# Kernel optimization log

Measured on AMD Instinct MI355X. Metric: run time of the kernel, lower is better.

## Reference

```python
import jax, jax.numpy as jnp
import numpy as np

N = 1536
F = 64          # in_features
F_IN = F + 1    # include_adj adds adjacency channel
OUT = 64


def setup_inputs() -> dict:
    key = jax.random.key(0)
    k1, k2, k3, k4 = jax.random.split(key, 4)
    feat = jax.random.normal(k1, (N, F), dtype=jnp.float32)
    adj = jax.random.uniform(k2, (N, N), dtype=jnp.float32)
    # nn.Linear init: U(-1/sqrt(fan_in), 1/sqrt(fan_in))
    bound = 1.0 / np.sqrt(F_IN)
    W = jax.random.uniform(k3, (OUT, F_IN), minval=-bound, maxval=bound, dtype=jnp.float32)
    b = jax.random.uniform(k4, (OUT,), minval=-bound, maxval=bound, dtype=jnp.float32)
    return {"feat": feat, "adj": adj, "W": W, "b": b}


def reference(feat, adj, W, b):
    # pairwise abs-diff via broadcasting (no repeat): [N, N, F]
    feat_diff = jnp.abs(feat[None, :, :] - feat[:, None, :])
    # concat adjacency as extra channel -> [N, N, F+1], then flatten rows
    x = jnp.concatenate([feat_diff, adj[:, :, None]], axis=2).reshape(N * N, F_IN)
    # Linear: x @ W.T + b -> [N*N, OUT]
    return x @ W.T + b
```

## Files before the change

### kernel.cpp

```cpp
#include <hip/hip_runtime.h>
#include <hip/hip_bf16.h>

#define N_NODES 1536
#define NF 64
#define NOUT 64
#define FIN 65
#define TI 6

typedef __bf16 bf16x8 __attribute__((ext_vector_type(8)));
typedef float f32x4 __attribute__((ext_vector_type(4)));

__global__ __launch_bounds__(256, 4)
void edge_gcn_mfma(const float* __restrict__ feat,
                   const float* __restrict__ adj,
                   const float* __restrict__ W,
                   const float* __restrict__ b,
                   float* __restrict__ out)
{
    const int tid  = threadIdx.x;
    const int lane = tid & 63;
    const int wv   = tid >> 6;
    const int l15  = lane & 15;
    const int lg   = lane >> 4;

    const int i0 = blockIdx.y * TI;
    const int j0 = blockIdx.x * 128;
    const int jw = j0 + wv * 32;

    __shared__ float lds[8192];
    __shared__ float fslab[TI * NF];
    __shared__ float aslab[TI * 128];
    float* const lbase = lds + wv * 2048;

    if (tid < 96) {
        const int row = tid >> 4;
        const int col = (tid & 15) * 4;
        *reinterpret_cast<f32x4*>(&fslab[row * NF + col]) =
            *reinterpret_cast<const f32x4*>(
                &feat[(size_t)(i0 + row) * NF + col]);
    }
    if (tid < 192) {
        const int row = tid >> 5;
        const int col = (tid & 31) * 4;
        *reinterpret_cast<f32x4*>(&aslab[row * 128 + col]) =
            *reinterpret_cast<const f32x4*>(
                &adj[(size_t)(i0 + row) * N_NODES + j0 + col]);
    }

    bf16x8 afrag[2][4];
#pragma unroll
    for (int kk = 0; kk < 2; ++kk) {
#pragma unroll
        for (int mo = 0; mo < 4; ++mo) {
            const float* wp = W + (mo * 16 + l15) * FIN + kk * 32 + lg * 8;
#pragma unroll
            for (int e = 0; e < 8; ++e) afrag[kk][mo][e] = (__bf16)wp[e];
        }
    }

    bf16x8 fjrb[2][2];
#pragma unroll
    for (int n = 0; n < 2; ++n) {
        const float* fjrow = feat + (jw + n * 16 + l15) * NF;
#pragma unroll
        for (int kk = 0; kk < 2; ++kk)
#pragma unroll
            for (int e = 0; e < 8; ++e)
                fjrb[n][kk][e] = (__bf16)fjrow[kk * 32 + lg * 8 + e];
    }

    float wlB[4], bvB[4];
#pragma unroll
    for (int r = 0; r < 4; ++r) {
        wlB[r] = W[(l15 * 4 + r) * FIN + NF];
        bvB[r] = b[l15 * 4 + r];
    }

    __syncthreads();

#pragma unroll 1
    for (int ii = 0; ii < TI; ++ii) {
        const int i = i0 + ii;

        bf16x8 fib[2];
#pragma unroll
        for (int kk = 0; kk < 2; ++kk) {
            const float* fp = &fslab[ii * NF + kk * 32 + lg * 8];
#pragma unroll
            for (int e = 0; e < 8; ++e) fib[kk][e] = (__bf16)fp[e];
        }

        f32x4 acc[4][2];
#pragma unroll
        for (int mo = 0; mo < 4; ++mo)
#pragma unroll
            for (int n = 0; n < 2; ++n)
                acc[mo][n] = (f32x4){0.f, 0.f, 0.f, 0.f};

#pragma unroll
        for (int n = 0; n < 2; ++n) {
#pragma unroll
            for (int kk = 0; kk < 2; ++kk) {
                bf16x8 bfrag;
#pragma unroll
                for (int e = 0; e < 8; ++e)
                    bfrag[e] = (__bf16)fabsf((float)fjrb[n][kk][e] -
                                             (float)fib[kk][e]);
#pragma unroll
                for (int mo = 0; mo < 4; ++mo)
                    acc[mo][n] = __builtin_amdgcn_mfma_f32_16x16x32_bf16(
                        afrag[kk][mo], bfrag, acc[mo][n], 0, 0, 0);
            }
        }

#pragma unroll
        for (int n = 0; n < 2; ++n) {
            const int jrow = n * 16 + l15;
#pragma unroll
            for (int mo = 0; mo < 4; ++mo) {
                const int swz = (mo * 16 + lg * 4) ^ ((l15 & 7) << 2);
                *reinterpret_cast<f32x4*>(lbase + jrow * 64 + swz) = acc[mo][n];
            }
        }

#pragma unroll
        for (int t = 0; t < 8; ++t) {
            const int jr = t * 4 + lg;
            const int oo = l15 * 4;
            f32x4 v = *reinterpret_cast<const f32x4*>(
                lbase + jr * 64 + (oo ^ ((jr & 7) << 2)));
            const float av = aslab[ii * 128 + wv * 32 + jr];
#pragma unroll
            for (int r = 0; r < 4; ++r)
                v[r] = v[r] + av * wlB[r] + bvB[r];
            float* op = out + ((size_t)i * N_NODES + jw + jr) * NOUT + oo;
            *reinterpret_cast<f32x4*>(op) = v;
        }
    }
}

extern "C" void kernel_launch(void* const* d_in, const int* in_sizes, int n_in,
                              void* d_out, int out_size, void* d_ws, size_t ws_size,
                              hipStream_t stream) {
    const float* feat = (const float*)d_in[0];
    const float* adj  = (const float*)d_in[1];
    const float* W    = (const float*)d_in[2];
    const float* b    = (const float*)d_in[3];
    float* out = (float*)d_out;

    dim3 grid(N_NODES / 128, N_NODES / TI);
    dim3 block(256);
    edge_gcn_mfma<<<grid, block, 0, stream>>>(feat, adj, W, b, out);
}
```

Before: 131.8 us.

## Specialize waves into MFMA producers and store consumers with double-buffered LDS

Splits each block into two compute waves, which run the MFMA tiles over 64 columns each, and two drain waves, which add the adjacency and bias terms and write the output from a double-buffered LDS tile one row behind. TI is doubled to 12 and launch bounds drop to 2 blocks per CU to make room for the larger LDS buffers and register tiles. The aim is to overlap the output stores, which dominate this kernel, with the MFMA compute. In exchange only half the waves issue stores, occupancy is lower, and a block barrier is added every row.

```diff
diff --git a/kernel.cpp b/kernel.cpp
--- a/kernel.cpp
+++ b/kernel.cpp
@@ -5,12 +5,12 @@
 #define NF 64
 #define NOUT 64
 #define FIN 65
-#define TI 6
+#define TI 12
 
 typedef __bf16 bf16x8 __attribute__((ext_vector_type(8)));
 typedef float f32x4 __attribute__((ext_vector_type(4)));
 
-__global__ __launch_bounds__(256, 4)
+__global__ __launch_bounds__(256, 2)
 void edge_gcn_mfma(const float* __restrict__ feat,
                    const float* __restrict__ adj,
                    const float* __restrict__ W,
@@ -25,118 +25,137 @@
 
     const int i0 = blockIdx.y * TI;
     const int j0 = blockIdx.x * 128;
-    const int jw = j0 + wv * 32;
 
-    __shared__ float lds[8192];
+    __shared__ float buf[2][128 * 64];
     __shared__ float fslab[TI * NF];
     __shared__ float aslab[TI * 128];
-    float* const lbase = lds + wv * 2048;
 
-    if (tid < 96) {
+    if (tid < 192) {
         const int row = tid >> 4;
         const int col = (tid & 15) * 4;
         *reinterpret_cast<f32x4*>(&fslab[row * NF + col]) =
             *reinterpret_cast<const f32x4*>(
                 &feat[(size_t)(i0 + row) * NF + col]);
     }
-    if (tid < 192) {
-        const int row = tid >> 5;
-        const int col = (tid & 31) * 4;
-        *reinterpret_cast<f32x4*>(&aslab[row * 128 + col]) =
-            *reinterpret_cast<const f32x4*>(
-                &adj[(size_t)(i0 + row) * N_NODES + j0 + col]);
+#pragma unroll
+    for (int h = 0; h < 2; ++h) {
+        const int idx = h * 256 + tid;
+        if (idx < 384) {
+            const int row = idx >> 5;
+            const int col = (idx & 31) * 4;
+            *reinterpret_cast<f32x4*>(&aslab[row * 128 + col]) =
+                *reinterpret_cast<const f32x4*>(
+                    &adj[(size_t)(i0 + row) * N_NODES + j0 + col]);
+        }
     }
 
     bf16x8 afrag[2][4];
-#pragma unroll
-    for (int kk = 0; kk < 2; ++kk) {
-#pragma unroll
-        for (int mo = 0; mo < 4; ++mo) {
-            const float* wp = W + (mo * 16 + l15) * FIN + kk * 32 + lg * 8;
-#pragma unroll
-            for (int e = 0; e < 8; ++e) afrag[kk][mo][e] = (__bf16)wp[e];
-        }
-    }
+    bf16x8 fjrb[4][2];
+    float wlB[4], bvB[4];
 
-    bf16x8 fjrb[2][2];
-#pragma unroll
-    for (int n = 0; n < 2; ++n) {
-        const float* fjrow = feat + (jw + n * 16 + l15) * NF;
+    if (wv < 2) {
+        const int cw = wv;
 #pragma unroll
         for (int kk = 0; kk < 2; ++kk)
 #pragma unroll
-            for (int e = 0; e < 8; ++e)
-                fjrb[n][kk][e] = (__bf16)fjrow[kk * 32 + lg * 8 + e];
-    }
-
-    float wlB[4], bvB[4];
+            for (int mo = 0; mo < 4; ++mo) {
+                const float* wp = W + (mo * 16 + l15) * FIN + kk * 32 + lg * 8;
 #pragma unroll
-    for (int r = 0; r < 4; ++r) {
-        wlB[r] = W[(l15 * 4 + r) * FIN + NF];
-        bvB[r] = b[l15 * 4 + r];
+                for (int e = 0; e < 8; ++e) afrag[kk][mo][e] = (__bf16)wp[e];
+            }
+#pragma unroll
+        for (int n = 0; n < 4; ++n) {
+            const float* fjrow =
+                feat + (size_t)(j0 + cw * 64 + n * 16 + l15) * NF;
+#pragma unroll
+            for (int kk = 0; kk < 2; ++kk)
+#pragma unroll
+                for (int e = 0; e < 8; ++e)
+                    fjrb[n][kk][e] = (__bf16)fjrow[kk * 32 + lg * 8 + e];
+        }
+    } else {
+#pragma unroll
+        for (int r = 0; r < 4; ++r) {
+            wlB[r] = W[(l15 * 4 + r) * FIN + NF];
+            bvB[r] = b[l15 * 4 + r];
+        }
     }
 
     __syncthreads();
 
-#pragma unroll 1
-    for (int ii = 0; ii < TI; ++ii) {
-        const int i = i0 + ii;
-
-        bf16x8 fib[2];
+    auto drain = [&](int jj) {
+        const int sw = wv - 2;
+        const float* lb = &buf[jj & 1][0];
+        float* const orow =
+            out + ((size_t)(i0 + jj) * N_NODES + j0 + sw * 64) * NOUT + l15 * 4;
 #pragma unroll
-        for (int kk = 0; kk < 2; ++kk) {
-            const float* fp = &fslab[ii * NF + kk * 32 + lg * 8];
-#pragma unroll
-            for (int e = 0; e < 8; ++e) fib[kk][e] = (__bf16)fp[e];
-        }
-
-        f32x4 acc[4][2];
-#pragma unroll
-        for (int mo = 0; mo < 4; ++mo)
-#pragma unroll
-            for (int n = 0; n < 2; ++n)
-                acc[mo][n] = (f32x4){0.f, 0.f, 0.f, 0.f};
-
-#pragma unroll
-        for (int n = 0; n < 2; ++n) {
-#pragma unroll
-            for (int kk = 0; kk < 2; ++kk) {
-                bf16x8 bfrag;
-#pragma unroll
-                for (int e = 0; e < 8; ++e)
-                    bfrag[e] = (__bf16)fabsf((float)fjrb[n][kk][e] -
-                                             (float)fib[kk][e]);
-#pragma unroll
-                for (int mo = 0; mo < 4; ++mo)
-                    acc[mo][n] = __builtin_amdgcn_mfma_f32_16x16x32_bf16(
-                        afrag[kk][mo], bfrag, acc[mo][n], 0, 0, 0);
-            }
-        }
-
-#pragma unroll
-        for (int n = 0; n < 2; ++n) {
-            const int jrow = n * 16 + l15;
-#pragma unroll
-            for (int mo = 0; mo < 4; ++mo) {
-                const int swz = (mo * 16 + lg * 4) ^ ((l15 & 7) << 2);
-                *reinterpret_cast<f32x4*>(lbase + jrow * 64 + swz) = acc[mo][n];
-            }
-        }
-
-#pragma unroll
-        for (int t = 0; t < 8; ++t) {
-            const int jr = t * 4 + lg;
-            const int oo = l15 * 4;
+        for (int t = 0; t < 16; ++t) {
+            const int jr  = t * 4 + lg;
+            const int row = sw * 64 + jr;
             f32x4 v = *reinterpret_cast<const f32x4*>(
-                lbase + jr * 64 + (oo ^ ((jr & 7) << 2)));
-            const float av = aslab[ii * 128 + wv * 32 + jr];
+                lb + row * 64 + ((l15 * 4) ^ ((row & 7) << 2)));
+            const float av = aslab[jj * 128 + row];
 #pragma unroll
             for (int r = 0; r < 4; ++r)
                 v[r] = v[r] + av * wlB[r] + bvB[r];
-            float* op = out + ((size_t)i * N_NODES + jw + jr) * NOUT + oo;
-            *reinterpret_cast<f32x4*>(op) = v;
+            *reinterpret_cast<f32x4*>(orow + jr * NOUT) = v;
         }
+    };
+
+#pragma unroll 1
+    for (int ii = 0; ii < TI; ++ii) {
+        if (wv < 2) {
+            const int cw = wv;
+            bf16x8 fib[2];
+#pragma unroll
+            for (int kk = 0; kk < 2; ++kk) {
+                const float* fp = &fslab[ii * NF + kk * 32 + lg * 8];
+#pragma unroll
+                for (int e = 0; e < 8; ++e) fib[kk][e] = (__bf16)fp[e];
+            }
+
+            f32x4 acc[4][4];
+#pragma unroll
+            for (int mo = 0; mo < 4; ++mo)
+#pragma unroll
+                for (int n = 0; n < 4; ++n)
+                    acc[mo][n] = (f32x4){0.f, 0.f, 0.f, 0.f};
+
+#pragma unroll
+            for (int n = 0; n < 4; ++n) {
+#pragma unroll
+                for (int kk = 0; kk < 2; ++kk) {
+                    bf16x8 bfrag;
+#pragma unroll
+                    for (int e = 0; e < 8; ++e)
+                        bfrag[e] = (__bf16)fabsf((float)fjrb[n][kk][e] -
+                                                 (float)fib[kk][e]);
+#pragma unroll
+                    for (int mo = 0; mo < 4; ++mo)
+                        acc[mo][n] = __builtin_amdgcn_mfma_f32_16x16x32_bf16(
+                            afrag[kk][mo], bfrag, acc[mo][n], 0, 0, 0);
+                }
+            }
+
+            float* lb = &buf[ii & 1][0];
+#pragma unroll
+            for (int n = 0; n < 4; ++n) {
+                const int row = cw * 64 + n * 16 + l15;
+#pragma unroll
+                for (int mo = 0; mo < 4; ++mo) {
+                    const int swz = (mo * 16 + lg * 4) ^ ((row & 7) << 2);
+                    *reinterpret_cast<f32x4*>(lb + row * 64 + swz) = acc[mo][n];
+                }
+            }
+        } else if (ii > 0) {
+            drain(ii - 1);
+        }
+
+        asm volatile("s_waitcnt lgkmcnt(0)" ::: "memory");
+        __builtin_amdgcn_sched_barrier(0);
+        __builtin_amdgcn_s_barrier();
     }
+    if (wv >= 2) drain(TI - 1);
 }
 
 extern "C" void kernel_launch(void* const* d_in, const int* in_sizes, int n_in,
```

Result: faster. 128.3 us (-2.6%).

## Assign one i-row per block and loop over j tiles with prefetched fj

Applied to the files above, without the earlier changes.

Changes the decomposition so each block handles a full row i (1536 blocks) and each wave loops over 12 j-tiles of 32. The fi fragment is loaded once and the fj features are software-pipelined through double-buffered registers. This is meant to hide global load latency for fj. In exchange, reuse of fj across several i rows is lost, register pressure rises, and launch bounds are relaxed to 3 waves per SIMD.

```diff
diff --git a/kernel.cpp b/kernel.cpp
--- a/kernel.cpp
+++ b/kernel.cpp
@@ -5,12 +5,11 @@
 #define NF 64
 #define NOUT 64
 #define FIN 65
-#define TI 6
 
 typedef __bf16 bf16x8 __attribute__((ext_vector_type(8)));
 typedef float f32x4 __attribute__((ext_vector_type(4)));
 
-__global__ __launch_bounds__(256, 4)
+__global__ __launch_bounds__(256, 3)
 void edge_gcn_mfma(const float* __restrict__ feat,
                    const float* __restrict__ adj,
                    const float* __restrict__ W,
@@ -23,50 +22,38 @@
     const int l15  = lane & 15;
     const int lg   = lane >> 4;
 
-    const int i0 = blockIdx.y * TI;
-    const int j0 = blockIdx.x * 128;
-    const int jw = j0 + wv * 32;
+    const int i  = blockIdx.x;
+    const int jw = wv * 384;
 
     __shared__ float lds[8192];
-    __shared__ float fslab[TI * NF];
-    __shared__ float aslab[TI * 128];
+    __shared__ float arow[N_NODES];
     float* const lbase = lds + wv * 2048;
 
-    if (tid < 96) {
-        const int row = tid >> 4;
-        const int col = (tid & 15) * 4;
-        *reinterpret_cast<f32x4*>(&fslab[row * NF + col]) =
-            *reinterpret_cast<const f32x4*>(
-                &feat[(size_t)(i0 + row) * NF + col]);
-    }
-    if (tid < 192) {
-        const int row = tid >> 5;
-        const int col = (tid & 31) * 4;
-        *reinterpret_cast<f32x4*>(&aslab[row * 128 + col]) =
-            *reinterpret_cast<const f32x4*>(
-                &adj[(size_t)(i0 + row) * N_NODES + j0 + col]);
+#pragma unroll
+    for (int h = 0; h < 2; ++h) {
+        const int idx = h * 256 + tid;
+        if (idx < 384)
+            *reinterpret_cast<f32x4*>(&arow[idx * 4]) =
+                *reinterpret_cast<const f32x4*>(
+                    &adj[(size_t)i * N_NODES + idx * 4]);
     }
 
     bf16x8 afrag[2][4];
 #pragma unroll
-    for (int kk = 0; kk < 2; ++kk) {
+    for (int kk = 0; kk < 2; ++kk)
 #pragma unroll
         for (int mo = 0; mo < 4; ++mo) {
             const float* wp = W + (mo * 16 + l15) * FIN + kk * 32 + lg * 8;
 #pragma unroll
             for (int e = 0; e < 8; ++e) afrag[kk][mo][e] = (__bf16)wp[e];
         }
-    }
 
-    bf16x8 fjrb[2][2];
+    bf16x8 fib[2];
 #pragma unroll
-    for (int n = 0; n < 2; ++n) {
-        const float* fjrow = feat + (jw + n * 16 + l15) * NF;
+    for (int kk = 0; kk < 2; ++kk) {
+        const float* fp = feat + (size_t)i * NF + kk * 32 + lg * 8;
 #pragma unroll
-        for (int kk = 0; kk < 2; ++kk)
-#pragma unroll
-            for (int e = 0; e < 8; ++e)
-                fjrb[n][kk][e] = (__bf16)fjrow[kk * 32 + lg * 8 + e];
+        for (int e = 0; e < 8; ++e) fib[kk][e] = (__bf16)fp[e];
     }
 
     float wlB[4], bvB[4];
@@ -78,17 +65,28 @@
 
     __syncthreads();
 
-#pragma unroll 1
-    for (int ii = 0; ii < TI; ++ii) {
-        const int i = i0 + ii;
+    auto load_fj = [&](bf16x8 fj[2][2], int it) {
+#pragma unroll
+        for (int n = 0; n < 2; ++n) {
+            const float* fjrow =
+                feat + (size_t)(jw + it * 32 + n * 16 + l15) * NF;
+#pragma unroll
+            for (int kk = 0; kk < 2; ++kk) {
+                f32x4 lo = *reinterpret_cast<const f32x4*>(
+                    fjrow + kk * 32 + lg * 8);
+                f32x4 hi = *reinterpret_cast<const f32x4*>(
+                    fjrow + kk * 32 + lg * 8 + 4);
+#pragma unroll
+                for (int e = 0; e < 4; ++e) {
+                    fj[n][kk][e]     = (__bf16)lo[e];
+                    fj[n][kk][e + 4] = (__bf16)hi[e];
+                }
+            }
+        }
+    };
 
-        bf16x8 fib[2];
-#pragma unroll
-        for (int kk = 0; kk < 2; ++kk) {
-            const float* fp = &fslab[ii * NF + kk * 32 + lg * 8];
-#pragma unroll
-            for (int e = 0; e < 8; ++e) fib[kk][e] = (__bf16)fp[e];
-        }
+    auto tile = [&](const bf16x8 fj[2][2], int it) {
+        const int jt = jw + it * 32;
 
         f32x4 acc[4][2];
 #pragma unroll
@@ -98,20 +96,19 @@
                 acc[mo][n] = (f32x4){0.f, 0.f, 0.f, 0.f};
 
 #pragma unroll
-        for (int n = 0; n < 2; ++n) {
+        for (int n = 0; n < 2; ++n)
 #pragma unroll
             for (int kk = 0; kk < 2; ++kk) {
                 bf16x8 bfrag;
 #pragma unroll
                 for (int e = 0; e < 8; ++e)
-                    bfrag[e] = (__bf16)fabsf((float)fjrb[n][kk][e] -
+                    bfrag[e] = (__bf16)fabsf((float)fj[n][kk][e] -
                                              (float)fib[kk][e]);
 #pragma unroll
                 for (int mo = 0; mo < 4; ++mo)
                     acc[mo][n] = __builtin_amdgcn_mfma_f32_16x16x32_bf16(
                         afrag[kk][mo], bfrag, acc[mo][n], 0, 0, 0);
             }
-        }
 
 #pragma unroll
         for (int n = 0; n < 2; ++n) {
@@ -129,13 +126,23 @@
             const int oo = l15 * 4;
             f32x4 v = *reinterpret_cast<const f32x4*>(
                 lbase + jr * 64 + (oo ^ ((jr & 7) << 2)));
-            const float av = aslab[ii * 128 + wv * 32 + jr];
+            const float av = arow[jt + jr];
 #pragma unroll
             for (int r = 0; r < 4; ++r)
                 v[r] = v[r] + av * wlB[r] + bvB[r];
-            float* op = out + ((size_t)i * N_NODES + jw + jr) * NOUT + oo;
+            float* op = out + ((size_t)i * N_NODES + jt + jr) * NOUT + oo;
             *reinterpret_cast<f32x4*>(op) = v;
         }
+    };
+
+    bf16x8 fjA[2][2], fjB[2][2];
+    load_fj(fjA, 0);
+#pragma unroll 1
+    for (int it = 0; it < 12; it += 2) {
+        load_fj(fjB, it + 1);
+        tile(fjA, it);
+        if (it + 2 < 12) load_fj(fjA, it + 2);
+        tile(fjB, it + 1);
     }
 }
 
@@ -148,7 +155,7 @@
     const float* b    = (const float*)d_in[3];
     float* out = (float*)d_out;
 
-    dim3 grid(N_NODES / 128, N_NODES / TI);
+    dim3 grid(N_NODES);
     dim3 block(256);
     edge_gcn_mfma<<<grid, block, 0, stream>>>(feat, adj, W, b, out);
 }
```

Measured after the change: 142.6 us. 8.2% more time.
